# Kernel optimization log

Measured on AMD Instinct MI355X. Metric: run time of the kernel, lower is better.

Reference implementation:

```python
import jax, jax.numpy as jnp
import numpy as np
import math

D_MODEL = 1024
NUM_HEADS = 16
SEQ = 2048
BATCH = 2


def setup_inputs() -> dict:
    key = jax.random.key(0)
    ks = jax.random.split(key, 12)
    s = 1.0 / math.sqrt(D_MODEL)
    inp = {
        "query": jax.random.normal(ks[0], (SEQ, BATCH, D_MODEL), jnp.float32),
        "key": jax.random.normal(ks[1], (SEQ, BATCH, D_MODEL), jnp.float32),
        "value": jax.random.normal(ks[2], (SEQ, BATCH, D_MODEL), jnp.float32),
        "Wq": jax.random.normal(ks[3], (D_MODEL, D_MODEL), jnp.float32) * s,
        "bq": jax.random.normal(ks[4], (D_MODEL,), jnp.float32) * 0.01,
        "Wk": jax.random.normal(ks[5], (D_MODEL, D_MODEL), jnp.float32) * s,
        "bk": jax.random.normal(ks[6], (D_MODEL,), jnp.float32) * 0.01,
        "Wv": jax.random.normal(ks[7], (D_MODEL, D_MODEL), jnp.float32) * s,
        "bv": jax.random.normal(ks[8], (D_MODEL,), jnp.float32) * 0.01,
        "Wo": jax.random.normal(ks[9], (D_MODEL, D_MODEL), jnp.float32) * s,
        "bo": jax.random.normal(ks[10], (D_MODEL,), jnp.float32) * 0.01,
    }
    # causal (subsequent) mask: True above the diagonal means masked
    inp["attn_mask"] = jnp.triu(jnp.ones((SEQ, SEQ), bool), k=1)
    # key_padding_mask: True = padding; random lengths in [SEQ//2, SEQ]
    lengths = jax.random.randint(ks[11], (BATCH,), SEQ // 2, SEQ + 1)
    inp["key_padding_mask"] = jnp.arange(SEQ)[None, :] >= lengths[:, None]
    return inp


def reference(query, key, value, Wq, bq, Wk, bk, Wv, bv, Wo, bo, attn_mask, key_padding_mask):
    S, B, D = query.shape
    H = NUM_HEADS
    dk = D // H

    def proj_split(x, W, b):
        y = x @ W.T + b                      # [S, B, D]
        return y.reshape(S, B, H, dk).transpose(1, 2, 0, 3)  # [B, H, S, dk]

    q = proj_split(query, Wq, bq)
    k = proj_split(key, Wk, bk)
    v = proj_split(value, Wv, bv)

    scores = jnp.einsum("bhqd,bhkd->bhqk", q, k) / jnp.sqrt(jnp.float32(dk))
    mask = key_padding_mask[:, None, None, :] | attn_mask[None, None, :, :]
    scores = jnp.where(mask, -jnp.inf, scores)
    p = jax.nn.softmax(scores, axis=-1)       # [B, H, S, S]
    x = jnp.einsum("bhqk,bhkd->bhqd", p, v)   # [B, H, S, dk]
    x = x.transpose(2, 0, 1, 3).reshape(S, B, D)
    return x @ Wo.T + bo
```

## Files before the change

### kernel.cpp

```cpp
#include <hip/hip_runtime.h>
#include <hip/hip_bf16.h>

#define S_LEN 2048
#define BATCH 2
#define DMODEL 1024
#define NHEAD 16
#define DK 64

typedef __bf16 bf16_t;
typedef bf16_t bf16x4 __attribute__((ext_vector_type(4)));
typedef bf16_t bf16x8 __attribute__((ext_vector_type(8)));
typedef float floatx4 __attribute__((ext_vector_type(4)));

#define SEG  ((size_t)S_LEN * BATCH * DMODEL)
#define WSEG ((size_t)DMODEL * DMODEL)
#define CVT_TOT (3 * SEG + 4 * WSEG)

#define QSCALE 0.180336879f

__global__ void prep_lens(const unsigned char* __restrict__ am,
                          const unsigned char* __restrict__ kpm,
                          int* __restrict__ lens)
{
    __shared__ int stride_s;
    __shared__ int cnt[BATCH];
    const int t = threadIdx.x;
    if (t == 0) {
        int st;
        if (am[1]) st = 1;
        else if (am[2] | am[3]) st = 2;
        else st = 4;
        stride_s = st;
    }
    if (t < BATCH) cnt[t] = 0;
    __syncthreads();
    const int st = stride_s;
    for (int idx = t; idx < BATCH * S_LEN; idx += blockDim.x) {
        int nz = 0;
        for (int c = 0; c < st; c++) nz |= kpm[idx * st + c];
        if (nz) atomicAdd(&cnt[idx / S_LEN], 1);
    }
    __syncthreads();
    if (t < BATCH) lens[t] = S_LEN - cnt[t];
}

__global__ void cvt_all(const float* __restrict__ q, const float* __restrict__ k,
                        const float* __restrict__ v, const float* __restrict__ wq,
                        const float* __restrict__ wk, const float* __restrict__ wv,
                        const float* __restrict__ wo, bf16_t* __restrict__ out)
{
    size_t i4 = ((size_t)blockIdx.x * blockDim.x + threadIdx.x) * 4;
    const size_t stride = (size_t)gridDim.x * blockDim.x * 4;
    for (; i4 < CVT_TOT; i4 += stride) {
        const float* src;
        size_t off;
        if (i4 < SEG)                    { src = q;  off = i4; }
        else if (i4 < 2 * SEG)           { src = k;  off = i4 - SEG; }
        else if (i4 < 3 * SEG)           { src = v;  off = i4 - 2 * SEG; }
        else if (i4 < 3 * SEG + WSEG)    { src = wq; off = i4 - 3 * SEG; }
        else if (i4 < 3 * SEG + 2 * WSEG){ src = wk; off = i4 - (3 * SEG + WSEG); }
        else if (i4 < 3 * SEG + 3 * WSEG){ src = wv; off = i4 - (3 * SEG + 2 * WSEG); }
        else                             { src = wo; off = i4 - (3 * SEG + 3 * WSEG); }
        const float4 x = *(const float4*)(src + off);
        bf16x4 r;
        r[0] = (bf16_t)x.x; r[1] = (bf16_t)x.y; r[2] = (bf16_t)x.z; r[3] = (bf16_t)x.w;
        *(bf16x4*)(out + i4) = r;
    }
}

__global__ __launch_bounds__(256, 2)
void gemm_qkv(const bf16_t* __restrict__ Abase, const bf16_t* __restrict__ Wbase,
              const float* __restrict__ bq, const float* __restrict__ bk,
              const float* __restrict__ bv, bf16_t* __restrict__ Obase)
{
    __shared__ bf16_t As[128 * 32];
    __shared__ bf16_t Bs[128 * 32];

    const int z = blockIdx.z;
    const bf16_t* A = Abase + (size_t)z * SEG;
    const bf16_t* W = Wbase + (size_t)z * WSEG;
    const float* bias = (z == 0) ? bq : (z == 1) ? bk : bv;
    bf16_t* C = Obase + (size_t)z * SEG;

    const int t    = threadIdx.x;
    const int wave = t >> 6;
    const int lane = t & 63;
    const int l15  = lane & 15;
    const int quad = lane >> 4;

    const int mBase = blockIdx.y * 128;
    const int nBase = blockIdx.x * 128;
    const int wRow  = (wave >> 1) * 64;
    const int wCol  = (wave & 1) * 64;

    floatx4 acc[4][4];
#pragma unroll
    for (int i = 0; i < 4; i++)
#pragma unroll
        for (int j = 0; j < 4; j++) acc[i][j] = (floatx4){0.f, 0.f, 0.f, 0.f};

    for (int k0 = 0; k0 < DMODEL; k0 += 32) {
#pragma unroll
        for (int c = 0; c < 2; c++) {
            const int chunk = c * 256 + t;
            const int row   = chunk >> 2;
            const int col   = (chunk & 3) * 8;
            const bf16_t* gA = A + (size_t)(mBase + row) * DMODEL + k0 + col;
            const bf16_t* gB = W + (size_t)(nBase + row) * DMODEL + k0 + col;
            bf16_t* lA = As + (c * 256 + wave * 64) * 8;
            bf16_t* lB = Bs + (c * 256 + wave * 64) * 8;
            __builtin_amdgcn_global_load_lds(
                (const __attribute__((address_space(1))) void*)gA,
                (__attribute__((address_space(3))) void*)lA, 16, 0, 0);
            __builtin_amdgcn_global_load_lds(
                (const __attribute__((address_space(1))) void*)gB,
                (__attribute__((address_space(3))) void*)lB, 16, 0, 0);
        }
        __syncthreads();

        bf16x8 af[4], bfr[4];
#pragma unroll
        for (int mi = 0; mi < 4; mi++)
            af[mi] = *(const bf16x8*)(As + (wRow + mi * 16 + l15) * 32 + quad * 8);
#pragma unroll
        for (int ni = 0; ni < 4; ni++)
            bfr[ni] = *(const bf16x8*)(Bs + (wCol + ni * 16 + l15) * 32 + quad * 8);
#pragma unroll
        for (int mi = 0; mi < 4; mi++)
#pragma unroll
            for (int ni = 0; ni < 4; ni++)
                acc[mi][ni] = __builtin_amdgcn_mfma_f32_16x16x32_bf16(
                    af[mi], bfr[ni], acc[mi][ni], 0, 0, 0);
        __syncthreads();
    }

    const float scale = (z == 0) ? QSCALE : 1.0f;
    float bvv[4];
#pragma unroll
    for (int ni = 0; ni < 4; ni++)
        bvv[ni] = bias[nBase + wCol + ni * 16 + l15];

#pragma unroll
    for (int mi = 0; mi < 4; mi++) {
#pragma unroll
        for (int ni = 0; ni < 4; ni++) {
            const int n = nBase + wCol + ni * 16 + l15;
            const int h = n >> 6, i = n & 63;
#pragma unroll
            for (int j = 0; j < 4; j++) {
                const int m = mBase + wRow + mi * 16 + quad * 4 + j;
                const int s = m >> 1, b = m & 1;
                const float v = (acc[mi][ni][j] + bvv[ni]) * scale;
                size_t off;
                if (z < 2)
                    off = ((size_t)(b * NHEAD + h) * S_LEN + s) * DK + i;
                else
                    off = ((size_t)(b * NHEAD + h) * DK + i) * S_LEN + s;
                C[off] = (bf16_t)v;
            }
        }
    }
}

__global__ __launch_bounds__(256, 4)
void attn(const bf16_t* __restrict__ qw, const bf16_t* __restrict__ kw,
          const bf16_t* __restrict__ vw, bf16_t* __restrict__ ow,
          const int* __restrict__ lens)
{
    __shared__ bf16_t Ks[2][64 * 64];
    __shared__ bf16_t Vs[2][64 * 64];
    __shared__ bf16_t Ps[4][16 * 64];

    const int t    = threadIdx.x;
    const int wave = t >> 6;
    const int lane = t & 63;
    const int l15  = lane & 15;
    const int quad = lane >> 4;
    const int qg   = lane & 48;
    const int rowbase = qg >> 2;

    const int n  = (int)(blockIdx.x + (blockIdx.y << 5));
    const int r  = n >> 8;
    const int j  = (n >> 3) & 31;
    const int bh = (n & 7) | (r << 3);
    const int flip  = (r == 1) | (r == 2);
    const int qTile = flip ? (31 - j) : j;
    const int b     = bh >> 4;
    const int len   = lens[b];
    const int qBase = qTile * 64;

    const bf16_t* kbase = kw + (size_t)bh * S_LEN * DK;
    const bf16_t* vbase = vw + (size_t)bh * DK * S_LEN;

    const int dr = lane >> 3;
    const int cc = (lane & 7) ^ dr;

    const bf16_t* Qg = qw + ((size_t)bh * S_LEN + qBase + wave * 16) * DK;
    const bf16x8 qa0 = *(const bf16x8*)(Qg + l15 * DK + quad * 8);
    const bf16x8 qa1 = *(const bf16x8*)(Qg + l15 * DK + 32 + quad * 8);

    floatx4 O[4];
#pragma unroll
    for (int i = 0; i < 4; i++) O[i] = (floatx4){0.f, 0.f, 0.f, 0.f};
    float lrow = 0.f;

    const int ktEnd = min(qTile, (len - 1) >> 6);

    auto dma_tile = [&](int ktB, int buf) {
#pragma unroll
        for (int i = 0; i < 2; i++) {
            const int R0 = (wave * 2 + i) * 8;
            const bf16_t* gK = kbase + (size_t)(ktB + R0 + dr) * DK + cc * 8;
            const bf16_t* gV = vbase + (size_t)(R0 + dr) * S_LEN + ktB + cc * 8;
            bf16_t* lK = &Ks[buf][(size_t)R0 * 64];
            bf16_t* lV = &Vs[buf][(size_t)R0 * 64];
            __builtin_amdgcn_global_load_lds(
                (const __attribute__((address_space(1))) void*)gK,
                (__attribute__((address_space(3))) void*)lK, 16, 0, 0);
            __builtin_amdgcn_global_load_lds(
                (const __attribute__((address_space(1))) void*)gV,
                (__attribute__((address_space(3))) void*)lV, 16, 0, 0);
        }
    };

    dma_tile(0, 0);
    __syncthreads();

    const int sw  = l15 & 7;
    const int ch0 = (quad ^ sw) * 8;
    const int ch1 = ((4 | quad) ^ sw) * 8;

    for (int kt = 0; kt <= ktEnd; kt++) {
        const int cur = kt & 1;
        if (kt < ktEnd) dma_tile((kt + 1) * 64, cur ^ 1);

        floatx4 sc[4];
#pragma unroll
        for (int ni = 0; ni < 4; ni++) {
            const bf16_t* kr = &Ks[cur][(ni * 16 + l15) * 64];
            const bf16x8 kf0 = *(const bf16x8*)(kr + ch0);
            const bf16x8 kf1 = *(const bf16x8*)(kr + ch1);
            floatx4 zz = (floatx4){0.f, 0.f, 0.f, 0.f};
            zz = __builtin_amdgcn_mfma_f32_16x16x32_bf16(kf0, qa0, zz, 0, 0, 0);
            zz = __builtin_amdgcn_mfma_f32_16x16x32_bf16(kf1, qa1, zz, 0, 0, 0);
            sc[ni] = zz;
        }

        const int ktBase = kt * 64;
        const int q = qBase + wave * 16 + l15;
        const bool needMask = (kt == qTile) || (ktBase + 64 > len);
        if (needMask) {
#pragma unroll
            for (int ni = 0; ni < 4; ni++) {
#pragma unroll
                for (int rr = 0; rr < 4; rr++) {
                    const int key = ktBase + ni * 16 + quad * 4 + rr;
                    if (key > q || key >= len) sc[ni][rr] = -3.0e38f;
                }
            }
        }

        float lsum = 0.f;
#pragma unroll
        for (int ni = 0; ni < 4; ni++) {
#pragma unroll
            for (int rr = 0; rr < 4; rr++) {
                const float p = exp2f(sc[ni][rr]);
                sc[ni][rr] = p;
                lsum += p;
            }
        }
        lrow += lsum;

        bf16_t* Pw = Ps[wave];
#pragma unroll
        for (int ni = 0; ni < 4; ni++) {
            bf16x4 pk;
            pk[0] = (bf16_t)sc[ni][0]; pk[1] = (bf16_t)sc[ni][1];
            pk[2] = (bf16_t)sc[ni][2]; pk[3] = (bf16_t)sc[ni][3];
            const int lc = 2 * ni + (quad >> 1);
            *(bf16x4*)(Pw + l15 * 64 + ((lc ^ sw) << 3) + (quad & 1) * 4) = pk;
        }

        const bf16x8 pa0 = *(const bf16x8*)(Pw + l15 * 64 + ((quad ^ sw) << 3));
        const bf16x8 pa1 = *(const bf16x8*)(Pw + l15 * 64 + (((4 | quad) ^ sw) << 3));
#pragma unroll
        for (int nd = 0; nd < 4; nd++) {
            const bf16_t* vr = &Vs[cur][(nd * 16 + l15) * 64];
            const bf16x8 vb0 = *(const bf16x8*)(vr + ch0);
            const bf16x8 vb1 = *(const bf16x8*)(vr + ch1);
            O[nd] = __builtin_amdgcn_mfma_f32_16x16x32_bf16(pa0, vb0, O[nd], 0, 0, 0);
            O[nd] = __builtin_amdgcn_mfma_f32_16x16x32_bf16(pa1, vb1, O[nd], 0, 0, 0);
        }
        __syncthreads();
    }

    lrow += __shfl_xor(lrow, 16);
    lrow += __shfl_xor(lrow, 32);

    float rinv[4];
#pragma unroll
    for (int jj = 0; jj < 4; jj++)
        rinv[jj] = 1.0f / __shfl(lrow, qg | (rowbase + jj));
#pragma unroll
    for (int nd = 0; nd < 4; nd++) {
        const int d = (bh & 15) * DK + nd * 16 + l15;
#pragma unroll
        for (int jj = 0; jj < 4; jj++) {
            const int qq = qBase + wave * 16 + quad * 4 + jj;
            ow[((size_t)qq * BATCH + b) * DMODEL + d] = (bf16_t)(O[nd][jj] * rinv[jj]);
        }
    }
}

__global__ __launch_bounds__(256, 2)
void gemm_o(const bf16_t* __restrict__ A, const bf16_t* __restrict__ W,
            const float* __restrict__ bias, float* __restrict__ C)
{
    __shared__ bf16_t As[128 * 32];
    __shared__ bf16_t Bs[64 * 32];

    const int t    = threadIdx.x;
    const int wave = t >> 6;
    const int lane = t & 63;
    const int l15  = lane & 15;
    const int quad = lane >> 4;

    const int mBase = blockIdx.y * 128;
    const int nBase = blockIdx.x * 64;
    const int wRow  = wave * 32;

    floatx4 acc[2][4];
#pragma unroll
    for (int i = 0; i < 2; i++)
#pragma unroll
        for (int j = 0; j < 4; j++) acc[i][j] = (floatx4){0.f, 0.f, 0.f, 0.f};

    for (int k0 = 0; k0 < DMODEL; k0 += 32) {
#pragma unroll
        for (int c = 0; c < 2; c++) {
            const int chunk = c * 256 + t;
            const int row   = chunk >> 2;
            const int col   = (chunk & 3) * 8;
            const bf16_t* gA = A + (size_t)(mBase + row) * DMODEL + k0 + col;
            bf16_t* lA = As + (c * 256 + wave * 64) * 8;
            __builtin_amdgcn_global_load_lds(
                (const __attribute__((address_space(1))) void*)gA,
                (__attribute__((address_space(3))) void*)lA, 16, 0, 0);
        }
        {
            const int row = t >> 2;
            const int col = (t & 3) * 8;
            const bf16_t* gB = W + (size_t)(nBase + row) * DMODEL + k0 + col;
            bf16_t* lB = Bs + (wave * 64) * 8;
            __builtin_amdgcn_global_load_lds(
                (const __attribute__((address_space(1))) void*)gB,
                (__attribute__((address_space(3))) void*)lB, 16, 0, 0);
        }
        __syncthreads();

        bf16x8 af[2], bfr[4];
#pragma unroll
        for (int mi = 0; mi < 2; mi++)
            af[mi] = *(const bf16x8*)(As + (wRow + mi * 16 + l15) * 32 + quad * 8);
#pragma unroll
        for (int ni = 0; ni < 4; ni++)
            bfr[ni] = *(const bf16x8*)(Bs + (ni * 16 + l15) * 32 + quad * 8);
#pragma unroll
        for (int mi = 0; mi < 2; mi++)
#pragma unroll
            for (int ni = 0; ni < 4; ni++)
                acc[mi][ni] = __builtin_amdgcn_mfma_f32_16x16x32_bf16(
                    af[mi], bfr[ni], acc[mi][ni], 0, 0, 0);
        __syncthreads();
    }

    float bvv[4];
#pragma unroll
    for (int ni = 0; ni < 4; ni++)
        bvv[ni] = bias[nBase + ni * 16 + l15];

#pragma unroll
    for (int mi = 0; mi < 2; mi++) {
#pragma unroll
        for (int ni = 0; ni < 4; ni++) {
            const int n = nBase + ni * 16 + l15;
#pragma unroll
            for (int j = 0; j < 4; j++) {
                const int m = mBase + wRow + mi * 16 + quad * 4 + j;
                C[(size_t)m * DMODEL + n] = acc[mi][ni][j] + bvv[ni];
            }
        }
    }
}

extern "C" void kernel_launch(void* const* d_in, const int* in_sizes, int n_in,
                              void* d_out, int out_size, void* d_ws, size_t ws_size,
                              hipStream_t stream)
{
    const float* query = (const float*)d_in[0];
    const float* key   = (const float*)d_in[1];
    const float* value = (const float*)d_in[2];
    const float* Wq = (const float*)d_in[3];
    const float* bq = (const float*)d_in[4];
    const float* Wk = (const float*)d_in[5];
    const float* bk = (const float*)d_in[6];
    const float* Wv = (const float*)d_in[7];
    const float* bv = (const float*)d_in[8];
    const float* Wo = (const float*)d_in[9];
    const float* bo = (const float*)d_in[10];
    const unsigned char* am  = (const unsigned char*)d_in[11];
    const unsigned char* kpm = (const unsigned char*)d_in[12];

    bf16_t* cvt   = (bf16_t*)d_ws;
    bf16_t* q_bf  = cvt;
    bf16_t* wq_bf = cvt + 3 * SEG;
    bf16_t* wo_bf = wq_bf + 3 * WSEG;
    bf16_t* q_ws  = cvt + CVT_TOT;
    bf16_t* k_ws  = q_ws + SEG;
    bf16_t* v_ws  = k_ws + SEG;
    bf16_t* o_ws  = q_bf;
    int*    lens  = (int*)(v_ws + SEG);

    prep_lens<<<1, 256, 0, stream>>>(am, kpm, lens);
    cvt_all<<<4096, 256, 0, stream>>>(query, key, value, Wq, Wk, Wv, Wo, cvt);

    gemm_qkv<<<dim3(DMODEL / 128, (S_LEN * BATCH) / 128, 3), dim3(256), 0, stream>>>(
        q_bf, wq_bf, bq, bk, bv, q_ws);

    attn<<<dim3(32, BATCH * NHEAD), dim3(256), 0, stream>>>(
        q_ws, k_ws, v_ws, o_ws, lens);

    gemm_o<<<dim3(DMODEL / 64, (S_LEN * BATCH) / 128), dim3(256), 0, stream>>>(
        o_ws, wo_bf, bo, (float*)d_out);
}
```

Before: 244.3 us.

## Swizzle GEMM LDS tiles, remap blocks per XCD, fuse mask-length prep into convert

Applies an XOR swizzle to the LDS column chunks in both projection GEMMs to cut bank conflicts on the fragment reads. Remaps block indices so each XCD works on a contiguous band of M rows, which should improve L2 reuse. Folds the key-padding length computation into extra blocks of the convert kernel, replacing a single-block launch that used shared-memory atomics with wave-shuffle reductions. Raises the minimum-occupancy hint on gemm_qkv to 3, which may cause register pressure or spills.

```diff
diff --git a/kernel.cpp b/kernel.cpp
--- a/kernel.cpp
+++ b/kernel.cpp
@@ -15,42 +15,45 @@
 #define SEG  ((size_t)S_LEN * BATCH * DMODEL)
 #define WSEG ((size_t)DMODEL * DMODEL)
 #define CVT_TOT (3 * SEG + 4 * WSEG)
+#define CVT_BLOCKS 4096
 
 #define QSCALE 0.180336879f
 
-__global__ void prep_lens(const unsigned char* __restrict__ am,
-                          const unsigned char* __restrict__ kpm,
-                          int* __restrict__ lens)
+__global__ void cvt_all(const float* __restrict__ q, const float* __restrict__ k,
+                        const float* __restrict__ v, const float* __restrict__ wq,
+                        const float* __restrict__ wk, const float* __restrict__ wv,
+                        const float* __restrict__ wo, bf16_t* __restrict__ out,
+                        const unsigned char* __restrict__ am,
+                        const unsigned char* __restrict__ kpm,
+                        int* __restrict__ lens)
 {
-    __shared__ int stride_s;
-    __shared__ int cnt[BATCH];
-    const int t = threadIdx.x;
-    if (t == 0) {
+    if (blockIdx.x >= CVT_BLOCKS) {
+        const int b = (int)blockIdx.x - CVT_BLOCKS;
+        __shared__ int cnt;
+        const int t = threadIdx.x;
+        if (t == 0) cnt = 0;
         int st;
         if (am[1]) st = 1;
         else if (am[2] | am[3]) st = 2;
         else st = 4;
-        stride_s = st;
-    }
-    if (t < BATCH) cnt[t] = 0;
-    __syncthreads();
-    const int st = stride_s;
-    for (int idx = t; idx < BATCH * S_LEN; idx += blockDim.x) {
-        int nz = 0;
-        for (int c = 0; c < st; c++) nz |= kpm[idx * st + c];
-        if (nz) atomicAdd(&cnt[idx / S_LEN], 1);
-    }
-    __syncthreads();
-    if (t < BATCH) lens[t] = S_LEN - cnt[t];
-}
-
-__global__ void cvt_all(const float* __restrict__ q, const float* __restrict__ k,
-                        const float* __restrict__ v, const float* __restrict__ wq,
-                        const float* __restrict__ wk, const float* __restrict__ wv,
-                        const float* __restrict__ wo, bf16_t* __restrict__ out)
-{
+        __syncthreads();
+        int local = 0;
+        for (int idx = t; idx < S_LEN; idx += blockDim.x) {
+            int nz = 0;
+            for (int c = 0; c < st; c++) nz |= kpm[(b * S_LEN + idx) * st + c];
+            local += (nz != 0);
+        }
+        local += __shfl_xor(local, 1);  local += __shfl_xor(local, 2);
+        local += __shfl_xor(local, 4);  local += __shfl_xor(local, 8);
+        local += __shfl_xor(local, 16); local += __shfl_xor(local, 32);
+        if ((t & 63) == 0) atomicAdd(&cnt, local);
+        __syncthreads();
+        if (t == 0) lens[b] = S_LEN - cnt;
+        return;
+    }
+
     size_t i4 = ((size_t)blockIdx.x * blockDim.x + threadIdx.x) * 4;
-    const size_t stride = (size_t)gridDim.x * blockDim.x * 4;
+    const size_t stride = (size_t)CVT_BLOCKS * blockDim.x * 4;
     for (; i4 < CVT_TOT; i4 += stride) {
         const float* src;
         size_t off;
@@ -68,7 +71,7 @@
     }
 }
 
-__global__ __launch_bounds__(256, 2)
+__global__ __launch_bounds__(256, 3)
 void gemm_qkv(const bf16_t* __restrict__ Abase, const bf16_t* __restrict__ Wbase,
               const float* __restrict__ bq, const float* __restrict__ bk,
               const float* __restrict__ bv, bf16_t* __restrict__ Obase)
@@ -76,7 +79,13 @@
     __shared__ bf16_t As[128 * 32];
     __shared__ bf16_t Bs[128 * 32];
 
-    const int z = blockIdx.z;
+    const int L   = (int)(blockIdx.x + (blockIdx.y << 3) + (blockIdx.z << 8));
+    const int xcd = L & 7;
+    const int w   = L >> 3;
+    const int z   = w >> 5;
+    const int mBase = ((xcd << 2) | (w & 3)) * 128;
+    const int nBase = ((w >> 2) & 7) * 128;
+
     const bf16_t* A = Abase + (size_t)z * SEG;
     const bf16_t* W = Wbase + (size_t)z * WSEG;
     const float* bias = (z == 0) ? bq : (z == 1) ? bk : bv;
@@ -88,10 +97,9 @@
     const int l15  = lane & 15;
     const int quad = lane >> 4;
 
-    const int mBase = blockIdx.y * 128;
-    const int nBase = blockIdx.x * 128;
     const int wRow  = (wave >> 1) * 64;
     const int wCol  = (wave & 1) * 64;
+    const int psw   = (l15 >> 1) & 3;
 
     floatx4 acc[4][4];
 #pragma unroll
@@ -104,9 +112,9 @@
         for (int c = 0; c < 2; c++) {
             const int chunk = c * 256 + t;
             const int row   = chunk >> 2;
-            const int col   = (chunk & 3) * 8;
-            const bf16_t* gA = A + (size_t)(mBase + row) * DMODEL + k0 + col;
-            const bf16_t* gB = W + (size_t)(nBase + row) * DMODEL + k0 + col;
+            const int lc    = ((chunk & 3) ^ ((row >> 1) & 3)) * 8;
+            const bf16_t* gA = A + (size_t)(mBase + row) * DMODEL + k0 + lc;
+            const bf16_t* gB = W + (size_t)(nBase + row) * DMODEL + k0 + lc;
             bf16_t* lA = As + (c * 256 + wave * 64) * 8;
             bf16_t* lB = Bs + (c * 256 + wave * 64) * 8;
             __builtin_amdgcn_global_load_lds(
@@ -121,10 +129,12 @@
         bf16x8 af[4], bfr[4];
 #pragma unroll
         for (int mi = 0; mi < 4; mi++)
-            af[mi] = *(const bf16x8*)(As + (wRow + mi * 16 + l15) * 32 + quad * 8);
+            af[mi] = *(const bf16x8*)(As + (wRow + mi * 16 + l15) * 32
+                                         + ((quad ^ psw)) * 8);
 #pragma unroll
         for (int ni = 0; ni < 4; ni++)
-            bfr[ni] = *(const bf16x8*)(Bs + (wCol + ni * 16 + l15) * 32 + quad * 8);
+            bfr[ni] = *(const bf16x8*)(Bs + (wCol + ni * 16 + l15) * 32
+                                          + ((quad ^ psw)) * 8);
 #pragma unroll
         for (int mi = 0; mi < 4; mi++)
 #pragma unroll
@@ -320,15 +330,20 @@
     __shared__ bf16_t As[128 * 32];
     __shared__ bf16_t Bs[64 * 32];
 
+    const int L   = (int)(blockIdx.x + (blockIdx.y << 4));
+    const int xcd = L & 7;
+    const int w   = L >> 3;
+    const int mBase = ((xcd << 2) | (w & 3)) * 128;
+    const int nBase = (w >> 2) * 64;
+
     const int t    = threadIdx.x;
     const int wave = t >> 6;
     const int lane = t & 63;
     const int l15  = lane & 15;
     const int quad = lane >> 4;
 
-    const int mBase = blockIdx.y * 128;
-    const int nBase = blockIdx.x * 64;
     const int wRow  = wave * 32;
+    const int psw   = (l15 >> 1) & 3;
 
     floatx4 acc[2][4];
 #pragma unroll
@@ -341,8 +356,8 @@
         for (int c = 0; c < 2; c++) {
             const int chunk = c * 256 + t;
             const int row   = chunk >> 2;
-            const int col   = (chunk & 3) * 8;
-            const bf16_t* gA = A + (size_t)(mBase + row) * DMODEL + k0 + col;
+            const int lc    = ((chunk & 3) ^ ((row >> 1) & 3)) * 8;
+            const bf16_t* gA = A + (size_t)(mBase + row) * DMODEL + k0 + lc;
             bf16_t* lA = As + (c * 256 + wave * 64) * 8;
             __builtin_amdgcn_global_load_lds(
                 (const __attribute__((address_space(1))) void*)gA,
@@ -350,8 +365,8 @@
         }
         {
             const int row = t >> 2;
-            const int col = (t & 3) * 8;
-            const bf16_t* gB = W + (size_t)(nBase + row) * DMODEL + k0 + col;
+            const int lc  = ((t & 3) ^ ((row >> 1) & 3)) * 8;
+            const bf16_t* gB = W + (size_t)(nBase + row) * DMODEL + k0 + lc;
             bf16_t* lB = Bs + (wave * 64) * 8;
             __builtin_amdgcn_global_load_lds(
                 (const __attribute__((address_space(1))) void*)gB,
@@ -362,10 +377,12 @@
         bf16x8 af[2], bfr[4];
 #pragma unroll
         for (int mi = 0; mi < 2; mi++)
-            af[mi] = *(const bf16x8*)(As + (wRow + mi * 16 + l15) * 32 + quad * 8);
+            af[mi] = *(const bf16x8*)(As + (wRow + mi * 16 + l15) * 32
+                                         + ((quad ^ psw)) * 8);
 #pragma unroll
         for (int ni = 0; ni < 4; ni++)
-            bfr[ni] = *(const bf16x8*)(Bs + (ni * 16 + l15) * 32 + quad * 8);
+            bfr[ni] = *(const bf16x8*)(Bs + (ni * 16 + l15) * 32
+                                          + ((quad ^ psw)) * 8);
 #pragma unroll
         for (int mi = 0; mi < 2; mi++)
 #pragma unroll
@@ -422,8 +439,8 @@
     bf16_t* o_ws  = q_bf;
     int*    lens  = (int*)(v_ws + SEG);
 
-    prep_lens<<<1, 256, 0, stream>>>(am, kpm, lens);
-    cvt_all<<<4096, 256, 0, stream>>>(query, key, value, Wq, Wk, Wv, Wo, cvt);
+    cvt_all<<<CVT_BLOCKS + BATCH, 256, 0, stream>>>(
+        query, key, value, Wq, Wk, Wv, Wo, cvt, am, kpm, lens);
 
     gemm_qkv<<<dim3(DMODEL / 128, (S_LEN * BATCH) / 128, 3), dim3(256), 0, stream>>>(
         q_bf, wq_bf, bq, bk, bv, q_ws);
```

Measured after the change: 228.3 us. 1.07x faster.
